# Performance work log

Hardware: AMD Instinct MI355X
Metric: run time of the kernel (lower is better)

## Reference

```python
import jax, jax.numpy as jnp
import numpy as np

N_NODES = 50000
IN_F = 512
OUT_F = 512
N_EDGES = 1600000
DROP_P = 0.5
NEG_SLOPE = 0.01  # torch LeakyReLU default


def leaky_relu(x):
    return jnp.where(x >= 0, x, NEG_SLOPE * x)


def setup_inputs() -> dict:
    key = jax.random.key(0)
    k1, k2, k3, k4, k5, k6 = jax.random.split(key, 6)
    x = jax.random.normal(k1, (N_NODES, IN_F), dtype=jnp.float32)
    W = jax.random.normal(k2, (OUT_F, IN_F), dtype=jnp.float32) * (1.0 / np.sqrt(IN_F))
    # inverted dropout mask: bernoulli(keep)/keep, keep = 1 - p
    keep = 1.0 - DROP_P
    drop_mask = (jax.random.uniform(k3, (N_NODES, IN_F)) < keep).astype(jnp.float32) / keep
    adj_vals = jax.random.uniform(k4, (N_EDGES,), dtype=jnp.float32)
    adj_rows = jax.random.randint(k5, (N_EDGES,), 0, N_NODES, dtype=jnp.int32)
    adj_cols = jax.random.randint(k6, (N_EDGES,), 0, N_NODES, dtype=jnp.int32)
    return {"x": x, "W": W, "drop_mask": drop_mask, "adj_vals": adj_vals,
            "adj_rows": adj_rows, "adj_cols": adj_cols}


def reference(x, W, drop_mask, adj_vals, adj_rows, adj_cols):
    # support = Linear(dropout(x)); Linear weight is [out, in] (torch convention)
    support = jnp.einsum('ni,oi->no', x * drop_mask, W)  # [N, out]
    h = leaky_relu(support)
    # sparse adj @ h: out[r] += v * h[c]
    msgs = adj_vals[:, None] * h[adj_cols]               # [E, out]
    agg = jax.ops.segment_sum(msgs, adj_rows, num_segments=N_NODES)
    return leaky_relu(agg)
```

## Files before the change

### kernel.cpp

```cpp
#include <hip/hip_runtime.h>

#define NROWS 50000
#define NFEAT 512
#define NEDGE 1600000
#define SLOPE 0.01f

typedef unsigned short u16;
typedef __attribute__((ext_vector_type(8))) short short8;
typedef __attribute__((ext_vector_type(4))) float f32x4;
typedef __attribute__((ext_vector_type(8))) unsigned short u16x8;

__device__ __forceinline__ u16 f2bf(float f) {
  unsigned u = __float_as_uint(f);
  u += 0x7fffu + ((u >> 16) & 1u);
  return (u16)(u >> 16);
}
__device__ __forceinline__ float lrelu(float v) { return v >= 0.f ? v : SLOPE * v; }

__device__ __forceinline__ void gload_lds16(const u16* g, u16* l) {
  __builtin_amdgcn_global_load_lds((const __attribute__((address_space(1))) void*)g,
                                   (__attribute__((address_space(3))) void*)l, 16, 0, 0);
}

__global__ void prep_kernel(const float* __restrict__ x, const float* __restrict__ m,
                            u16* __restrict__ xd, const float* __restrict__ w,
                            u16* __restrict__ wb, const int* __restrict__ rows,
                            int* __restrict__ counts) {
  const int stride = gridDim.x * blockDim.x;
  const int tid0 = blockIdx.x * blockDim.x + threadIdx.x;
  for (int i = tid0; i < (NROWS * NFEAT) / 8; i += stride) {
    size_t b = (size_t)i * 2;
    float4 a0 = ((const float4*)x)[b], a1 = ((const float4*)x)[b + 1];
    float4 m0 = ((const float4*)m)[b], m1 = ((const float4*)m)[b + 1];
    u16x8 o;
    o[0] = f2bf(a0.x * m0.x); o[1] = f2bf(a0.y * m0.y);
    o[2] = f2bf(a0.z * m0.z); o[3] = f2bf(a0.w * m0.w);
    o[4] = f2bf(a1.x * m1.x); o[5] = f2bf(a1.y * m1.y);
    o[6] = f2bf(a1.z * m1.z); o[7] = f2bf(a1.w * m1.w);
    *(u16x8*)(xd + (size_t)i * 8) = o;
  }
  for (int i = tid0; i < (NFEAT * NFEAT) / 8; i += stride) {
    size_t b = (size_t)i * 2;
    float4 a0 = ((const float4*)w)[b], a1 = ((const float4*)w)[b + 1];
    u16x8 o;
    o[0] = f2bf(a0.x); o[1] = f2bf(a0.y); o[2] = f2bf(a0.z); o[3] = f2bf(a0.w);
    o[4] = f2bf(a1.x); o[5] = f2bf(a1.y); o[6] = f2bf(a1.z); o[7] = f2bf(a1.w);
    *(u16x8*)(wb + (size_t)i * 8) = o;
  }
  for (int e = tid0; e < NEDGE; e += stride) atomicAdd(&counts[rows[e]], 1);
}

__global__ void scan_kernel(const int* __restrict__ counts, int* __restrict__ offs) {
  __shared__ int wpre[17];
  const int t = threadIdx.x;
  const int lane = t & 63, w = t >> 6;
  const int CH = (NROWS + 1023) / 1024;
  int beg = t * CH; if (beg > NROWS) beg = NROWS;
  int end = beg + CH; if (end > NROWS) end = NROWS;
  int s = 0;
  for (int i = beg; i < end; ++i) s += counts[i];
  int inc = s;
#pragma unroll
  for (int d = 1; d < 64; d <<= 1) {
    int u = __shfl_up(inc, d);
    if (lane >= d) inc += u;
  }
  if (lane == 63) wpre[w + 1] = inc;
  __syncthreads();
  if (t == 0) {
    wpre[0] = 0;
    for (int i = 1; i <= 16; ++i) wpre[i] += wpre[i - 1];
    offs[NROWS] = wpre[16];
  }
  __syncthreads();
  int run = wpre[w] + inc - s;
  for (int i = beg; i < end; ++i) { offs[i] = run; run += counts[i]; }
}

__global__ void scatter_kernel(const float* __restrict__ vals, const int* __restrict__ rows,
                               const int* __restrict__ cols, const int* __restrict__ offs,
                               int* __restrict__ cursor, int2* __restrict__ svc) {
  int stride = gridDim.x * blockDim.x;
  for (int e = blockIdx.x * blockDim.x + threadIdx.x; e < NEDGE; e += stride) {
    int r = rows[e];
    int p = offs[r] + atomicAdd(&cursor[r], 1);
    int2 q;
    q.x = __float_as_int(vals[e]);
    q.y = cols[e];
    svc[p] = q;
  }
}

__global__ __launch_bounds__(256) void gemm_kernel(const u16* __restrict__ xd,
                                                   const u16* __restrict__ wb,
                                                   unsigned char* __restrict__ hq,
                                                   float* __restrict__ scaleg) {
  __shared__ __align__(16) u16 lAB[2 * 128 * 32];
  __shared__ float wmax[2][128];
  __shared__ float rinv[128];
  u16* lA = lAB;
  u16* lB = lAB + 128 * 32;
  const int tid = threadIdx.x;
  const int lane = tid & 63;
  const int wid = tid >> 6;
  const int wm = wid >> 1, wn = wid & 1;
  const int bx = blockIdx.x;
  const int tm = bx >> 2;
  const int tn = bx & 3;
  const long rowBase = (long)tm * 128;

  f32x4 acc[4][4] = {};

  const int srow = lane >> 2;
  const int skoff = (lane & 3) * 8;

  for (int k0 = 0; k0 < 512; k0 += 32) {
    __syncthreads();
#pragma unroll
    for (int i = 0; i < 2; ++i) {
      int rowA = wid * 32 + i * 16 + srow;
      long gr = rowBase + rowA;
      if (gr > NROWS - 1) gr = NROWS - 1;
      gload_lds16(xd + gr * 512 + k0 + skoff, lA + (wid * 32 + i * 16) * 32);
      int rowB = wid * 32 + i * 16 + srow;
      gload_lds16(wb + ((long)tn * 128 + rowB) * 512 + k0 + skoff,
                  lB + (wid * 32 + i * 16) * 32);
    }
    __syncthreads();
    short8 a[4], b[4];
    const int rsel = lane & 15, ksel = (lane >> 4) * 8;
#pragma unroll
    for (int m = 0; m < 4; ++m)
      a[m] = *(const short8*)(lA + (wm * 64 + m * 16 + rsel) * 32 + ksel);
#pragma unroll
    for (int n = 0; n < 4; ++n)
      b[n] = *(const short8*)(lB + (wn * 64 + n * 16 + rsel) * 32 + ksel);
#pragma unroll
    for (int m = 0; m < 4; ++m)
#pragma unroll
      for (int n = 0; n < 4; ++n)
        acc[m][n] = __builtin_amdgcn_mfma_f32_16x16x32_bf16(a[m], b[n], acc[m][n], 0, 0, 0);
  }

  const int crow = (lane >> 4) * 4;
  const int ccol = lane & 15;

  float pm[4][4];
#pragma unroll
  for (int m = 0; m < 4; ++m)
#pragma unroll
    for (int r2 = 0; r2 < 4; ++r2) {
      float mx = 0.f;
#pragma unroll
      for (int n = 0; n < 4; ++n) mx = fmaxf(mx, fabsf(lrelu(acc[m][n][r2])));
      pm[m][r2] = mx;
    }
#pragma unroll
  for (int d = 1; d < 16; d <<= 1)
#pragma unroll
    for (int m = 0; m < 4; ++m)
#pragma unroll
      for (int r2 = 0; r2 < 4; ++r2) pm[m][r2] = fmaxf(pm[m][r2], __shfl_xor(pm[m][r2], d));
  if ((lane & 15) == 0) {
#pragma unroll
    for (int m = 0; m < 4; ++m)
#pragma unroll
      for (int r2 = 0; r2 < 4; ++r2) wmax[wn][wm * 64 + m * 16 + crow + r2] = pm[m][r2];
  }
  __syncthreads();
  if (tid < 128) {
    float rm = fmaxf(wmax[0][tid], wmax[1][tid]);
    float s = rm > 0.f ? rm * (1.f / 127.f) : 1.f;
    rinv[tid] = rm > 0.f ? 127.f / rm : 0.f;
    long gr = rowBase + tid;
    if (gr < NROWS) scaleg[gr * 4 + tn] = s;
  }
  __syncthreads();

  unsigned char* lT = (unsigned char*)lAB;
#pragma unroll
  for (int m = 0; m < 4; ++m) {
    int row0 = wm * 64 + m * 16 + crow;
    float ri0 = rinv[row0], ri1 = rinv[row0 + 1], ri2 = rinv[row0 + 2], ri3 = rinv[row0 + 3];
#pragma unroll
    for (int n = 0; n < 4; ++n) {
      int col = wn * 64 + n * 16 + ccol;
      float q0 = rintf(lrelu(acc[m][n][0]) * ri0);
      float q1 = rintf(lrelu(acc[m][n][1]) * ri1);
      float q2 = rintf(lrelu(acc[m][n][2]) * ri2);
      float q3 = rintf(lrelu(acc[m][n][3]) * ri3);
      int i0 = min(127, max(-127, (int)q0));
      int i1 = min(127, max(-127, (int)q1));
      int i2 = min(127, max(-127, (int)q2));
      int i3 = min(127, max(-127, (int)q3));
      unsigned pk = (i0 & 0xff) | ((i1 & 0xff) << 8) | ((i2 & 0xff) << 16) | ((i3 & 0xff) << 24);
#pragma unroll
      for (int r2 = 0; r2 < 4; ++r2) {
        int row = row0 + r2;
        lT[row * 128 + (col ^ ((row & 7) << 4))] = (unsigned char)(pk >> (8 * r2));
      }
    }
  }
  __syncthreads();
  {
    const int row = tid >> 1, seg = tid & 1;
    long gr = rowBase + row;
    if (gr < NROWS) {
      unsigned char* dst = hq + gr * 512 + tn * 128;
#pragma unroll
      for (int j = 0; j < 4; ++j) {
        int s = seg * 4 + j;
        int4 vv = *(const int4*)(lT + row * 128 + ((s ^ (row & 7)) << 4));
        *(int4*)(dst + s * 16) = vv;
      }
    }
  }
}

__global__ __launch_bounds__(256) void aggregate_kernel(const unsigned char* __restrict__ hq,
                                                        const float* __restrict__ scaleg,
                                                        const int2* __restrict__ svc,
                                                        const int* __restrict__ offs,
                                                        float* __restrict__ out) {
  const int lane = threadIdx.x & 63;
  const int wid = threadIdx.x >> 6;
  const int r = blockIdx.x * 4 + wid;
  if (r >= NROWS) return;
  const int beg = offs[r], end = offs[r + 1];
  const int grp = lane >> 4;
  float a[8] = {};
  const unsigned char* hp = hq + lane * 8;
  int2 cb[8], nb[8];
  const int ng = (end - beg) >> 3;
  if (ng > 0) {
#pragma unroll
    for (int k = 0; k < 8; ++k) cb[k] = svc[beg + k];
  }
  for (int g = 0; g < ng; ++g) {
    if (g + 1 < ng) {
#pragma unroll
      for (int k = 0; k < 8; ++k) nb[k] = svc[beg + (g + 1) * 8 + k];
    }
#pragma unroll
    for (int k = 0; k < 8; ++k) {
      float v = __int_as_float(cb[k].x);
      size_t c = (size_t)cb[k].y;
      float vs = v * scaleg[c * 4 + grp];
      uint2 q = *(const uint2*)(hp + c * 512);
      a[0] += vs * (float)(signed char)(q.x);
      a[1] += vs * (float)(signed char)(q.x >> 8);
      a[2] += vs * (float)(signed char)(q.x >> 16);
      a[3] += vs * (float)(signed char)(q.x >> 24);
      a[4] += vs * (float)(signed char)(q.y);
      a[5] += vs * (float)(signed char)(q.y >> 8);
      a[6] += vs * (float)(signed char)(q.y >> 16);
      a[7] += vs * (float)(signed char)(q.y >> 24);
    }
    if (g + 1 < ng) {
#pragma unroll
      for (int k = 0; k < 8; ++k) cb[k] = nb[k];
    }
  }
  for (int e = beg + ng * 8; e < end; ++e) {
    int2 q2 = svc[e];
    float v = __int_as_float(q2.x);
    size_t c = (size_t)q2.y;
    float vs = v * scaleg[c * 4 + grp];
    uint2 q = *(const uint2*)(hp + c * 512);
    a[0] += vs * (float)(signed char)(q.x);
    a[1] += vs * (float)(signed char)(q.x >> 8);
    a[2] += vs * (float)(signed char)(q.x >> 16);
    a[3] += vs * (float)(signed char)(q.x >> 24);
    a[4] += vs * (float)(signed char)(q.y);
    a[5] += vs * (float)(signed char)(q.y >> 8);
    a[6] += vs * (float)(signed char)(q.y >> 16);
    a[7] += vs * (float)(signed char)(q.y >> 24);
  }
  float* op = out + (size_t)r * NFEAT + lane * 8;
  float4 o0, o1;
  o0.x = lrelu(a[0]); o0.y = lrelu(a[1]); o0.z = lrelu(a[2]); o0.w = lrelu(a[3]);
  o1.x = lrelu(a[4]); o1.y = lrelu(a[5]); o1.z = lrelu(a[6]); o1.w = lrelu(a[7]);
  *(float4*)op = o0;
  *(float4*)(op + 4) = o1;
}

extern "C" void kernel_launch(void* const* d_in, const int* in_sizes, int n_in,
                              void* d_out, int out_size, void* d_ws, size_t ws_size,
                              hipStream_t stream) {
  const float* x = (const float*)d_in[0];
  const float* W = (const float*)d_in[1];
  const float* mask = (const float*)d_in[2];
  const float* vals = (const float*)d_in[3];
  const int* rows = (const int*)d_in[4];
  const int* cols = (const int*)d_in[5];
  float* out = (float*)d_out;
  char* ws = (char*)d_ws;

  const size_t o_xd = 0;
  const size_t o_hq = o_xd + 51200000;
  const size_t o_wb = o_hq + 25600000;
  const size_t o_scale = o_wb + 524288;
  const size_t o_counts = o_scale + 800000;
  const size_t o_cursor = o_counts + 200000;
  const size_t o_offs = o_cursor + 200000;
  const size_t o_svc = o_offs + 200064;

  u16* xd = (u16*)(ws + o_xd);
  unsigned char* hq = (unsigned char*)(ws + o_hq);
  u16* wb = (u16*)(ws + o_wb);
  float* scaleg = (float*)(ws + o_scale);
  int* counts = (int*)(ws + o_counts);
  int* cursor = (int*)(ws + o_cursor);
  int* offs = (int*)(ws + o_offs);
  int2* svc = (int2*)(ws + o_svc);

  hipMemsetAsync(counts, 0, 400000, stream);

  prep_kernel<<<2048, 256, 0, stream>>>(x, mask, xd, W, wb, rows, counts);
  scan_kernel<<<1, 1024, 0, stream>>>(counts, offs);
  scatter_kernel<<<2048, 256, 0, stream>>>(vals, rows, cols, offs, cursor, svc);
  gemm_kernel<<<391 * 4, 256, 0, stream>>>(xd, wb, hq, scaleg);
  aggregate_kernel<<<12500, 256, 0, stream>>>(hq, scaleg, svc, offs, out);
}
```

Baseline: 444.8 us.

## Vectorize CSR build, widen GEMM K-tile with swizzle, split aggregation across feature halves

The edge-count loop in prep and the scatter kernel now read rows, cols and vals as int4/float4, so each thread handles four edges. The scan is rewritten to use vectorized int4 loads and stores over 64-entry chunks. The GEMM moves to a K-tile of 64 with an XOR-swizzled LDS layout, which halves the number of barriers and is meant to avoid bank conflicts. Aggregation launches twice as many blocks, each wave covering half the features with 4-byte gathers per lane; this adds parallelism but rereads the edge list twice.

```diff
diff --git a/kernel.cpp b/kernel.cpp
--- a/kernel.cpp
+++ b/kernel.cpp
@@ -47,18 +47,32 @@
     o[4] = f2bf(a1.x); o[5] = f2bf(a1.y); o[6] = f2bf(a1.z); o[7] = f2bf(a1.w);
     *(u16x8*)(wb + (size_t)i * 8) = o;
   }
-  for (int e = tid0; e < NEDGE; e += stride) atomicAdd(&counts[rows[e]], 1);
+  for (int i = tid0; i < NEDGE / 4; i += stride) {
+    int4 r4 = ((const int4*)rows)[i];
+    atomicAdd(&counts[r4.x], 1);
+    atomicAdd(&counts[r4.y], 1);
+    atomicAdd(&counts[r4.z], 1);
+    atomicAdd(&counts[r4.w], 1);
+  }
 }
 
 __global__ void scan_kernel(const int* __restrict__ counts, int* __restrict__ offs) {
   __shared__ int wpre[17];
   const int t = threadIdx.x;
   const int lane = t & 63, w = t >> 6;
-  const int CH = (NROWS + 1023) / 1024;
-  int beg = t * CH; if (beg > NROWS) beg = NROWS;
-  int end = beg + CH; if (end > NROWS) end = NROWS;
+  const int beg = t * 64;
+  int4 c4[16];
   int s = 0;
-  for (int i = beg; i < end; ++i) s += counts[i];
+  if (beg < NROWS) {
+#pragma unroll
+    for (int g = 0; g < 16; ++g) {
+      int idx = beg + g * 4;
+      if (idx < NROWS) {
+        c4[g] = ((const int4*)counts)[idx >> 2];
+        s += c4[g].x + c4[g].y + c4[g].z + c4[g].w;
+      }
+    }
+  }
   int inc = s;
 #pragma unroll
   for (int d = 1; d < 64; d <<= 1) {
@@ -74,19 +88,39 @@
   }
   __syncthreads();
   int run = wpre[w] + inc - s;
-  for (int i = beg; i < end; ++i) { offs[i] = run; run += counts[i]; }
+  if (beg < NROWS) {
+#pragma unroll
+    for (int g = 0; g < 16; ++g) {
+      int idx = beg + g * 4;
+      if (idx < NROWS) {
+        int4 o;
+        o.x = run; run += c4[g].x;
+        o.y = run; run += c4[g].y;
+        o.z = run; run += c4[g].z;
+        o.w = run; run += c4[g].w;
+        ((int4*)offs)[idx >> 2] = o;
+      }
+    }
+  }
 }
 
 __global__ void scatter_kernel(const float* __restrict__ vals, const int* __restrict__ rows,
                                const int* __restrict__ cols, const int* __restrict__ offs,
                                int* __restrict__ cursor, int2* __restrict__ svc) {
-  int stride = gridDim.x * blockDim.x;
-  for (int e = blockIdx.x * blockDim.x + threadIdx.x; e < NEDGE; e += stride) {
-    int r = rows[e];
-    int p = offs[r] + atomicAdd(&cursor[r], 1);
+  int e0 = (blockIdx.x * blockDim.x + threadIdx.x) * 4;
+  if (e0 >= NEDGE) return;
+  int4 r4 = *(const int4*)(rows + e0);
+  int4 c4 = *(const int4*)(cols + e0);
+  float4 v4 = *(const float4*)(vals + e0);
+  int rr[4] = {r4.x, r4.y, r4.z, r4.w};
+  int cc[4] = {c4.x, c4.y, c4.z, c4.w};
+  float vv[4] = {v4.x, v4.y, v4.z, v4.w};
+#pragma unroll
+  for (int j = 0; j < 4; ++j) {
+    int p = offs[rr[j]] + atomicAdd(&cursor[rr[j]], 1);
     int2 q;
-    q.x = __float_as_int(vals[e]);
-    q.y = cols[e];
+    q.x = __float_as_int(vv[j]);
+    q.y = cc[j];
     svc[p] = q;
   }
 }
@@ -95,11 +129,11 @@
                                                    const u16* __restrict__ wb,
                                                    unsigned char* __restrict__ hq,
                                                    float* __restrict__ scaleg) {
-  __shared__ __align__(16) u16 lAB[2 * 128 * 32];
+  __shared__ __align__(16) u16 lAB[2 * 128 * 64];
   __shared__ float wmax[2][128];
   __shared__ float rinv[128];
   u16* lA = lAB;
-  u16* lB = lAB + 128 * 32;
+  u16* lB = lAB + 128 * 64;
   const int tid = threadIdx.x;
   const int lane = tid & 63;
   const int wid = tid >> 6;
@@ -111,35 +145,45 @@
 
   f32x4 acc[4][4] = {};
 
-  const int srow = lane >> 2;
-  const int skoff = (lane & 3) * 8;
-
-  for (int k0 = 0; k0 < 512; k0 += 32) {
+  const int sl8 = lane >> 3;
+  const int scol = ((lane & 7) ^ sl8) * 8;
+  const int rsel = lane & 15, kgrp = (lane >> 4) * 8;
+
+  for (int k0 = 0; k0 < 512; k0 += 64) {
     __syncthreads();
 #pragma unroll
-    for (int i = 0; i < 2; ++i) {
-      int rowA = wid * 32 + i * 16 + srow;
-      long gr = rowBase + rowA;
+    for (int c = 0; c < 4; ++c) {
+      int rbase = wid * 32 + c * 8;
+      long gr = rowBase + rbase + sl8;
       if (gr > NROWS - 1) gr = NROWS - 1;
-      gload_lds16(xd + gr * 512 + k0 + skoff, lA + (wid * 32 + i * 16) * 32);
-      int rowB = wid * 32 + i * 16 + srow;
-      gload_lds16(wb + ((long)tn * 128 + rowB) * 512 + k0 + skoff,
-                  lB + (wid * 32 + i * 16) * 32);
+      gload_lds16(xd + gr * 512 + k0 + scol, lA + rbase * 64);
+      gload_lds16(wb + ((long)tn * 128 + rbase + sl8) * 512 + k0 + scol, lB + rbase * 64);
     }
     __syncthreads();
-    short8 a[4], b[4];
-    const int rsel = lane & 15, ksel = (lane >> 4) * 8;
-#pragma unroll
-    for (int m = 0; m < 4; ++m)
-      a[m] = *(const short8*)(lA + (wm * 64 + m * 16 + rsel) * 32 + ksel);
-#pragma unroll
-    for (int n = 0; n < 4; ++n)
-      b[n] = *(const short8*)(lB + (wn * 64 + n * 16 + rsel) * 32 + ksel);
-#pragma unroll
-    for (int m = 0; m < 4; ++m)
-#pragma unroll
-      for (int n = 0; n < 4; ++n)
-        acc[m][n] = __builtin_amdgcn_mfma_f32_16x16x32_bf16(a[m], b[n], acc[m][n], 0, 0, 0);
+    short8 a[4][2], b[4][2];
+#pragma unroll
+    for (int m = 0; m < 4; ++m) {
+      int ar = wm * 64 + m * 16 + rsel;
+      const u16* base = lA + ar * 64;
+      int sw = (ar & 7) << 3;
+      a[m][0] = *(const short8*)(base + (kgrp ^ sw));
+      a[m][1] = *(const short8*)(base + ((32 + kgrp) ^ sw));
+    }
+#pragma unroll
+    for (int n = 0; n < 4; ++n) {
+      int br = wn * 64 + n * 16 + rsel;
+      const u16* base = lB + br * 64;
+      int sw = (br & 7) << 3;
+      b[n][0] = *(const short8*)(base + (kgrp ^ sw));
+      b[n][1] = *(const short8*)(base + ((32 + kgrp) ^ sw));
+    }
+#pragma unroll
+    for (int kk = 0; kk < 2; ++kk)
+#pragma unroll
+      for (int m = 0; m < 4; ++m)
+#pragma unroll
+        for (int n = 0; n < 4; ++n)
+          acc[m][n] = __builtin_amdgcn_mfma_f32_16x16x32_bf16(a[m][kk], b[n][kk], acc[m][n], 0, 0, 0);
   }
 
   const int crow = (lane >> 4) * 4;
@@ -224,12 +268,13 @@
                                                         float* __restrict__ out) {
   const int lane = threadIdx.x & 63;
   const int wid = threadIdx.x >> 6;
-  const int r = blockIdx.x * 4 + wid;
+  const int p = blockIdx.x / 12500;
+  const int r = (blockIdx.x % 12500) * 4 + wid;
   if (r >= NROWS) return;
   const int beg = offs[r], end = offs[r + 1];
-  const int grp = lane >> 4;
-  float a[8] = {};
-  const unsigned char* hp = hq + lane * 8;
+  const int grp = p * 2 + (lane >> 5);
+  float a0 = 0.f, a1 = 0.f, a2 = 0.f, a3 = 0.f;
+  const unsigned char* hp = hq + p * 256 + lane * 4;
   int2 cb[8], nb[8];
   const int ng = (end - beg) >> 3;
   if (ng > 0) {
@@ -246,15 +291,11 @@
       float v = __int_as_float(cb[k].x);
       size_t c = (size_t)cb[k].y;
       float vs = v * scaleg[c * 4 + grp];
-      uint2 q = *(const uint2*)(hp + c * 512);
-      a[0] += vs * (float)(signed char)(q.x);
-      a[1] += vs * (float)(signed char)(q.x >> 8);
-      a[2] += vs * (float)(signed char)(q.x >> 16);
-      a[3] += vs * (float)(signed char)(q.x >> 24);
-      a[4] += vs * (float)(signed char)(q.y);
-      a[5] += vs * (float)(signed char)(q.y >> 8);
-      a[6] += vs * (float)(signed char)(q.y >> 16);
-      a[7] += vs * (float)(signed char)(q.y >> 24);
+      unsigned q = *(const unsigned*)(hp + c * 512);
+      a0 += vs * (float)(signed char)(q);
+      a1 += vs * (float)(signed char)(q >> 8);
+      a2 += vs * (float)(signed char)(q >> 16);
+      a3 += vs * (float)(signed char)(q >> 24);
     }
     if (g + 1 < ng) {
 #pragma unroll
@@ -266,22 +307,15 @@
     float v = __int_as_float(q2.x);
     size_t c = (size_t)q2.y;
     float vs = v * scaleg[c * 4 + grp];
-    uint2 q = *(const uint2*)(hp + c * 512);
-    a[0] += vs * (float)(signed char)(q.x);
-    a[1] += vs * (float)(signed char)(q.x >> 8);
-    a[2] += vs * (float)(signed char)(q.x >> 16);
-    a[3] += vs * (float)(signed char)(q.x >> 24);
-    a[4] += vs * (float)(signed char)(q.y);
-    a[5] += vs * (float)(signed char)(q.y >> 8);
-    a[6] += vs * (float)(signed char)(q.y >> 16);
-    a[7] += vs * (float)(signed char)(q.y >> 24);
-  }
-  float* op = out + (size_t)r * NFEAT + lane * 8;
-  float4 o0, o1;
-  o0.x = lrelu(a[0]); o0.y = lrelu(a[1]); o0.z = lrelu(a[2]); o0.w = lrelu(a[3]);
-  o1.x = lrelu(a[4]); o1.y = lrelu(a[5]); o1.z = lrelu(a[6]); o1.w = lrelu(a[7]);
-  *(float4*)op = o0;
-  *(float4*)(op + 4) = o1;
+    unsigned q = *(const unsigned*)(hp + c * 512);
+    a0 += vs * (float)(signed char)(q);
+    a1 += vs * (float)(signed char)(q >> 8);
+    a2 += vs * (float)(signed char)(q >> 16);
+    a3 += vs * (float)(signed char)(q >> 24);
+  }
+  float4 o;
+  o.x = lrelu(a0); o.y = lrelu(a1); o.z = lrelu(a2); o.w = lrelu(a3);
+  *(float4*)(out + (size_t)r * NFEAT + p * 256 + lane * 4) = o;
 }
 
 extern "C" void kernel_launch(void* const* d_in, const int* in_sizes, int n_in,
@@ -318,7 +352,7 @@
 
   prep_kernel<<<2048, 256, 0, stream>>>(x, mask, xd, W, wb, rows, counts);
   scan_kernel<<<1, 1024, 0, stream>>>(counts, offs);
-  scatter_kernel<<<2048, 256, 0, stream>>>(vals, rows, cols, offs, cursor, svc);
+  scatter_kernel<<<1563, 256, 0, stream>>>(vals, rows, cols, offs, cursor, svc);
   gemm_kernel<<<391 * 4, 256, 0, stream>>>(xd, wb, hq, scaleg);
-  aggregate_kernel<<<12500, 256, 0, stream>>>(hq, scaleg, svc, offs, out);
-}
+  aggregate_kernel<<<25000, 256, 0, stream>>>(hq, scaleg, svc, offs, out);
+}
```

Measured after the change: 423.7 us. -4.7%, faster.
